# Kernel tuning notes

Measured on AMD Instinct MI355X. Metric: run time of the kernel, lower is better.

The kernel has to match this reference:

```python
import jax, jax.numpy as jnp
import numpy as np

N = 100000   # nodes
E = 800000   # edges
IN = 128     # in_dim
H = 256      # hidden
G = 512      # global cache rows


def _w(k, shape):
    fan_in = shape[0]
    return jax.random.normal(k, shape, jnp.float32) / np.sqrt(fan_in)


def setup_inputs() -> dict:
    key = jax.random.key(0)
    ks = jax.random.split(key, 24)
    x = jax.random.normal(ks[0], (N, IN), jnp.float32)
    edge_index = jax.random.randint(ks[1], (2, E), 0, N, jnp.int64)
    global_cache = jax.random.normal(ks[2], (G, H), jnp.float32)
    return {
        "x": x,
        "edge_index": edge_index,
        "global_cache": global_cache,
        "Wp": _w(ks[3], (IN, 64)), "bp": jnp.zeros((64,), jnp.float32),
        "W1l": _w(ks[4], (64, H)), "b1l": jnp.zeros((H,), jnp.float32),
        "W1r": _w(ks[5], (64, H)),
        "W2l": _w(ks[6], (H, H)), "b2l": jnp.zeros((H,), jnp.float32),
        "W2r": _w(ks[7], (H, H)),
        "Wq": _w(ks[8], (H, H)), "bq": jnp.zeros((H,), jnp.float32),
        "Wk": _w(ks[9], (H, H)), "bk": jnp.zeros((H,), jnp.float32),
        "Wv": _w(ks[10], (H, H)), "bv": jnp.zeros((H,), jnp.float32),
        "Wm1": _w(ks[11], (2 * H, H)), "bm1": jnp.zeros((H,), jnp.float32),
        "Wm2": _w(ks[12], (H, 2)), "bm2": jnp.zeros((2,), jnp.float32),
    }


def _sage(h, src, dst, Wl, bl, Wr):
    # PyG SAGEConv (mean aggr): lin_l(mean_{j in N(i)} h_j) + lin_r(h_i)
    agg = jax.ops.segment_sum(h[src], dst, num_segments=N)          # [N, d]
    cnt = jax.ops.segment_sum(jnp.ones((src.shape[0],), h.dtype), dst, num_segments=N)
    mean = agg / jnp.maximum(cnt, 1.0)[:, None]
    return mean @ Wl + bl + h @ Wr


def reference(x, edge_index, global_cache, Wp, bp, W1l, b1l, W1r,
              W2l, b2l, W2r, Wq, bq, Wk, bk, Wv, bv, Wm1, bm1, Wm2, bm2):
    src, dst = edge_index[0], edge_index[1]
    x_emb = jax.nn.relu(x @ Wp + bp)                                 # [N, 64]
    h = jax.nn.relu(_sage(x_emb, src, dst, W1l, b1l, W1r))           # [N, H]
    # dropout is identity in eval mode
    h = _sage(h, src, dst, W2l, b2l, W2r)                            # [N, H]
    # global attention
    Q = h @ Wq + bq                                                  # [N, H]
    K = global_cache @ Wk + bk                                       # [G, H]
    V = global_cache @ Wv + bv                                       # [G, H]
    attn = jax.nn.softmax(Q @ K.T / np.sqrt(H).astype(np.float32), axis=-1)  # [N, G]
    g = attn @ V                                                     # [N, H]
    h_cat = jnp.concatenate([h, g], axis=1)                          # [N, 2H]
    out = jax.nn.relu(h_cat @ Wm1 + bm1) @ Wm2 + bm2                 # [N, 2]
    return out
```

## Files before the change

kernel.cpp:

```cpp
#include <hip/hip_runtime.h>
#include <cstdint>
#include <cstddef>


#define NN 100000
#define NE 800000
#define CR 50000
#define NB1 98
#define CNTB 3125
#define XCVB 12500
#define NJOB 11
#define WCVB (NJOB * 32)
#define EMB_MB 782

typedef __attribute__((ext_vector_type(8))) short short8;
typedef __attribute__((ext_vector_type(8))) unsigned short ushort8;
typedef __attribute__((ext_vector_type(4))) float f32x4;

__device__ __forceinline__ float b2f(ushort u) {
  union { unsigned u; float f; } v; v.u = ((unsigned)u) << 16; return v.f;
}
__device__ __forceinline__ ushort f2b(float f) {
  union { float f; unsigned u; } v; v.f = f;
  unsigned r = v.u + 0x7FFFu + ((v.u >> 16) & 1u);
  return (ushort)(r >> 16);
}
__device__ __forceinline__ void gl_lds16(const void* g, void* l) {
  __builtin_amdgcn_global_load_lds((const __attribute__((address_space(1))) void*)g,
                                   (__attribute__((address_space(3))) void*)l, 16, 0, 0);
}

__global__ void zero_detect_k(const int* __restrict__ ei, int* __restrict__ flag,
                              int* __restrict__ cnt, int n) {
  if (blockIdx.x == 0) {
    __shared__ int ok;
    int t = threadIdx.x;
    if (t == 0) ok = 1;
    __syncthreads();
    if (ei[2 * t + 1] != 0) ok = 0;
    __syncthreads();
    if (t == 0) *flag = ok;
  } else {
    int i = (blockIdx.x - 1) * 256 + threadIdx.x;
    if (i < n) cnt[i] = 0;
  }
}

struct CvtJobs {
  const float* src[NJOB];
  ushort* dst[NJOB];
  int R[NJOB], C[NJOB], off[NJOB], tr[NJOB];
  float sc[NJOB];
};

__global__ void count_cvt_k(const int* __restrict__ ei, const int* __restrict__ flag,
                            int* __restrict__ cnt, int* __restrict__ loc,
                            const float* __restrict__ x, ushort* __restrict__ xb,
                            int E, int n4, CvtJobs jb) {
  int b = blockIdx.x;
  if (b < CNTB) {
    int i = b * 256 + threadIdx.x;
    if (i >= E) return;
    const bool i64 = (*flag != 0);
    unsigned d = (unsigned)(i64 ? ei[2 * E + 2 * i] : ei[E + i]);
    int p = -1;
    if (d < NN) p = atomicAdd(&cnt[d], 1);
    loc[i] = p;
  } else if (b < CNTB + XCVB) {
    int i = (b - CNTB) * 256 + threadIdx.x;
    if (i < n4) {
      float4 v = ((const float4*)x)[i];
      ushort4 o; o.x = f2b(v.x); o.y = f2b(v.y); o.z = f2b(v.z); o.w = f2b(v.w);
      ((ushort4*)xb)[i] = o;
    }
  } else {
    int wb = b - CNTB - XCVB;
    int j = wb >> 5;
    int ib = wb & 31;
    const int Cj = jb.C[j], Rj = jb.R[j];
    const float sc = jb.sc[j];
    const int n = Rj * Cj;
    if (jb.tr[j]) {
      for (int i = ib * 256 + threadIdx.x; i < n; i += 32 * 256) {
        int c = i / Rj, r = i - c * Rj;
        jb.dst[j][i] = f2b(jb.src[j][(size_t)(jb.off[j] + r) * Cj + c] * sc);
      }
    } else {
      for (int i = ib * 256 + threadIdx.x; i < n; i += 32 * 256)
        jb.dst[j][i] = f2b(jb.src[j][i] * sc);
    }
  }
}

__device__ __forceinline__ void scan1_body(const int* __restrict__ cnt,
                                           int* __restrict__ rowptr,
                                           int* __restrict__ bsum, int n, int b,
                                           char* smem) {
  int* ls = (int*)smem;
  const int t = threadIdx.x;
  const int base = b * 1024 + t * 4;
  int v[4]; int s = 0;
#pragma unroll
  for (int j = 0; j < 4; ++j) { int i = base + j; v[j] = (i < n) ? cnt[i] : 0; s += v[j]; }
  ls[t] = s; __syncthreads();
  int x = s;
  for (int o = 1; o < 256; o <<= 1) {
    int a = (t >= o) ? ls[t - o] : 0; __syncthreads();
    x += a; ls[t] = x; __syncthreads();
  }
  int run = x - s;
#pragma unroll
  for (int j = 0; j < 4; ++j) { run += v[j]; int i = base + j; if (i < n) rowptr[i + 1] = run; }
  if (t == 255) bsum[b] = x;
}

__device__ __forceinline__ void scan2_body(const int* __restrict__ bsum,
                                           int* __restrict__ boff, int nb,
                                           char* smem) {
  int* ls = (int*)smem;
  int t = threadIdx.x;
  int v = (t < 128 && t < nb) ? bsum[t] : 0;
  if (t < 128) ls[t] = v;
  __syncthreads();
  int x = v;
  for (int o = 1; o < 128; o <<= 1) {
    int a = (t < 128 && t >= o) ? ls[t - o] : 0;
    __syncthreads();
    x += a;
    if (t < 128) ls[t] = x;
    __syncthreads();
  }
  if (t < 128 && t < nb) boff[t] = x - v;
}

__device__ __forceinline__ void sbias_body(const float* __restrict__ bq,
                                           const ushort* __restrict__ Kmat,
                                           float* __restrict__ sbias, int blk) {
  int g = blk * 4 + (threadIdx.x >> 6);
  int lane = threadIdx.x & 63;
  if (g >= 512) return;
  ushort4 kv = ((const ushort4*)(Kmat + (size_t)g * 256))[lane];
  float4 bv = ((const float4*)bq)[lane];
  float p = b2f(kv.x) * bv.x + b2f(kv.y) * bv.y + b2f(kv.z) * bv.z + b2f(kv.w) * bv.w;
  for (int off = 32; off; off >>= 1) p += __shfl_xor(p, off);
  if (lane == 0) sbias[g] = p * 0.0625f;
}

__global__ void scan3_k(int* __restrict__ rowptr, const int* __restrict__ boff, int n) {
  int i = blockIdx.x * 256 + threadIdx.x;
  if (i == 0) rowptr[0] = 0;
  if (i < n) rowptr[i + 1] += boff[i >> 10];
}

__global__ void fill_edges_k(const int* __restrict__ ei, const int* __restrict__ flag,
                             const int* __restrict__ rowptr, const int* __restrict__ loc,
                             int* __restrict__ eidx, int E) {
  int i = blockIdx.x * 256 + threadIdx.x;
  if (i >= E) return;
  const bool i64 = (*flag != 0);
  unsigned s = (unsigned)(i64 ? ei[2 * i] : ei[i]);
  unsigned d = (unsigned)(i64 ? ei[2 * E + 2 * i] : ei[E + i]);
  int lc = loc[i];
  if (d < NN && s < NN && lc >= 0) {
    unsigned p = (unsigned)(rowptr[d] + lc);
    if (p < (unsigned)E) eidx[p] = (int)s;
  }
}

__global__ void agg64_k(const ushort* __restrict__ X, const int* __restrict__ rowptr,
                        const int* __restrict__ eidx, ushort* __restrict__ mean,
                        int r0, int M) {
  int nl = blockIdx.x * 4 + (threadIdx.x >> 6);
  int l = threadIdx.x & 63;
  int e4 = l >> 4;
  int d4 = l & 15;
  if (nl >= M) return;
  int node = r0 + nl;
  int s = rowptr[node], e = rowptr[node + 1];
  float a0 = 0.f, a1 = 0.f, a2 = 0.f, a3 = 0.f;
  for (int i = s + e4; i < e; i += 4) {
    unsigned sc = (unsigned)eidx[i];
    if (sc < NN) {
      ushort4 v = ((const ushort4*)(X + (size_t)sc * 64))[d4];
      a0 += b2f(v.x); a1 += b2f(v.y); a2 += b2f(v.z); a3 += b2f(v.w);
    }
  }
  a0 += __shfl_xor(a0, 16); a0 += __shfl_xor(a0, 32);
  a1 += __shfl_xor(a1, 16); a1 += __shfl_xor(a1, 32);
  a2 += __shfl_xor(a2, 16); a2 += __shfl_xor(a2, 32);
  a3 += __shfl_xor(a3, 16); a3 += __shfl_xor(a3, 32);
  if (e4 == 0) {
    float inv = 1.f / (float)max(e - s, 1);
    ushort4 o; o.x = f2b(a0 * inv); o.y = f2b(a1 * inv); o.z = f2b(a2 * inv); o.w = f2b(a3 * inv);
    ((ushort4*)(mean + (size_t)nl * 64))[d4] = o;
  }
}

__global__ void agg256_k(const ushort* __restrict__ X, const int* __restrict__ rowptr,
                         const int* __restrict__ eidx, ushort* __restrict__ mean,
                         int r0, int M) {
  int nl = blockIdx.x * 4 + (threadIdx.x >> 6);
  int l = threadIdx.x & 63;
  int g = l >> 5;
  int d = l & 31;
  if (nl >= M) return;
  int node = r0 + nl;
  int s = rowptr[node], e = rowptr[node + 1];
  float a[8], c[8];
#pragma unroll
  for (int k = 0; k < 8; ++k) { a[k] = 0.f; c[k] = 0.f; }
  for (int i = s + g; i < e; i += 4) {
    unsigned s0 = (unsigned)eidx[i];
    if (s0 < NN) {
      ushort8 v = *(const ushort8*)(X + (size_t)s0 * 256 + d * 8);
#pragma unroll
      for (int k = 0; k < 8; ++k) a[k] += b2f((ushort)v[k]);
    }
    int i2 = i + 2;
    if (i2 < e) {
      unsigned s1 = (unsigned)eidx[i2];
      if (s1 < NN) {
        ushort8 v = *(const ushort8*)(X + (size_t)s1 * 256 + d * 8);
#pragma unroll
        for (int k = 0; k < 8; ++k) c[k] += b2f((ushort)v[k]);
      }
    }
  }
  float inv = 1.f / (float)max(e - s, 1);
  ushort8 o;
#pragma unroll
  for (int k = 0; k < 8; ++k) {
    float t = a[k] + c[k];
    t += __shfl_xor(t, 32);
    o[k] = (short)f2b(t * inv);
  }
  if (g == 0) *(ushort8*)(mean + (size_t)nl * 256 + d * 8) = o;
}

template<int BN, bool RELU, bool OUTBF>
__device__ __forceinline__ void gemm_body(
    const ushort* __restrict__ A1, const ushort* __restrict__ BT1, int K1,
    const ushort* __restrict__ A2, const ushort* __restrict__ BT2, int K2,
    const float* __restrict__ bias, void* __restrict__ Cv, int M, int Nc,
    int bmi, int bni, char* smem) {
  constexpr int NR = BN / 32;
  constexpr int WTN = BN / 2;
  constexpr int ABYT = 128 * 64 * 2;
  constexpr int BBYT = BN * 64 * 2;
  constexpr int BUF = ABYT + BBYT;
  constexpr int CP = BN + 8;
  const int tid = threadIdx.x;
  const int l = tid & 63;
  const int w = tid >> 6;
  const int wm = w >> 1, wn = w & 1;
  const int bm = bmi * 128, bn = bni * BN;
  const int r15 = l & 15, g4 = l >> 4;

  const int nt1 = K1 >> 6;
  const int nt2 = A2 ? (K2 >> 6) : 0;
  const int nt = nt1 + nt2;

  auto STAGE = [&](int buf, int t) {
    const ushort* A = (t < nt1) ? A1 : A2;
    const ushort* BT = (t < nt1) ? BT1 : BT2;
    const int K = (t < nt1) ? K1 : K2;
    const int k0 = ((t < nt1) ? t : t - nt1) << 6;
    char* As = smem + buf * BUF;
    char* Bs = As + ABYT;
#pragma unroll
    for (int p = 0; p < 4; ++p) {
      int idx = tid + p * 256;
      int row = idx >> 3, slot = idx & 7;
      int kb = slot ^ (row & 7);
      int grow = bm + row; if (grow >= M) grow = M - 1;
      gl_lds16(A + (size_t)grow * K + k0 + kb * 8, As + idx * 16);
    }
#pragma unroll
    for (int p = 0; p < BN / 32; ++p) {
      int idx = tid + p * 256;
      int row = idx >> 3, slot = idx & 7;
      int kb = slot ^ (row & 7);
      gl_lds16(BT + (size_t)(bn + row) * K + k0 + kb * 8, Bs + idx * 16);
    }
  };

  f32x4 acc[4][NR];
  const f32x4 zz = {0.f, 0.f, 0.f, 0.f};
#pragma unroll
  for (int m = 0; m < 4; ++m)
#pragma unroll
    for (int n = 0; n < NR; ++n) acc[m][n] = zz;

  STAGE(0, 0);
  int cur = 0;
  for (int t = 0; t < nt; ++t) {
    __syncthreads();
    if (t + 1 < nt) STAGE(cur ^ 1, t + 1);
    const char* As = smem + cur * BUF;
    const char* Bs = As + ABYT;
#pragma unroll
    for (int s = 0; s < 2; ++s) {
      short8 a[4], b[NR];
      const int slotx = (((s * 4 + g4) ^ (r15 & 7)) << 4);
#pragma unroll
      for (int m = 0; m < 4; ++m) {
        int row = wm * 64 + m * 16 + r15;
        a[m] = *(const short8*)(As + row * 128 + slotx);
      }
#pragma unroll
      for (int n = 0; n < NR; ++n) {
        int row = wn * WTN + n * 16 + r15;
        b[n] = *(const short8*)(Bs + row * 128 + slotx);
      }
#pragma unroll
      for (int m = 0; m < 4; ++m)
#pragma unroll
        for (int n = 0; n < NR; ++n)
          acc[m][n] = __builtin_amdgcn_mfma_f32_16x16x32_bf16(a[m], b[n], acc[m][n], 0, 0, 0);
    }
    cur ^= 1;
  }
  __syncthreads();
  if (OUTBF) {
    ushort* Cs = (ushort*)smem;
#pragma unroll
    for (int n = 0; n < NR; ++n) {
      int col = wn * WTN + n * 16 + r15;
      float bv = bias ? bias[bn + col] : 0.f;
#pragma unroll
      for (int m = 0; m < 4; ++m) {
#pragma unroll
        for (int j = 0; j < 4; ++j) {
          int row = wm * 64 + m * 16 + g4 * 4 + j;
          float v = acc[m][n][j] + bv;
          if (RELU) v = fmaxf(v, 0.f);
          Cs[row * CP + col] = f2b(v);
        }
      }
    }
    __syncthreads();
    constexpr int C8 = BN / 8;
    for (int it = tid; it < 128 * C8; it += 256) {
      int row = it / C8, c8 = it % C8;
      if (bm + row < M)
        *(ushort8*)((ushort*)Cv + (size_t)(bm + row) * Nc + bn + c8 * 8) =
            *(const ushort8*)(Cs + row * CP + c8 * 8);
    }
  } else {
#pragma unroll
    for (int n = 0; n < NR; ++n) {
      int col = bn + wn * WTN + n * 16 + r15;
      float bv = bias ? bias[col] : 0.f;
#pragma unroll
      for (int m = 0; m < 4; ++m) {
#pragma unroll
        for (int j = 0; j < 4; ++j) {
          int row = bm + wm * 64 + m * 16 + g4 * 4 + j;
          if (row < M) {
            float v = acc[m][n][j] + bv;
            if (RELU) v = fmaxf(v, 0.f);
            ((float*)Cv)[(size_t)row * Nc + col] = v;
          }
        }
      }
    }
  }
}

template<int BN, bool RELU, bool OUTBF>
__global__ __launch_bounds__(256)
void mfma_gemm_k(const ushort* __restrict__ A1, const ushort* __restrict__ BT1, int K1,
                 const ushort* __restrict__ A2, const ushort* __restrict__ BT2, int K2,
                 const float* __restrict__ bias, void* __restrict__ Cv, int M, int Nc) {
  constexpr int BUF = 128 * 64 * 2 + BN * 64 * 2;
  constexpr int CP = BN + 8;
  constexpr int SZ_EPI = 128 * CP * 2;
  constexpr int SZ = (2 * BUF > SZ_EPI) ? 2 * BUF : SZ_EPI;
  __shared__ __align__(16) char smem[SZ];
  gemm_body<BN, RELU, OUTBF>(A1, BT1, K1, A2, BT2, K2, bias, Cv, M, Nc,
                             blockIdx.x, blockIdx.y, smem);
}

__global__ __launch_bounds__(256)
void stage2_k(const int* __restrict__ cnt, int* __restrict__ rowptr, int* __restrict__ bsum,
              const ushort* __restrict__ gcb, const ushort* __restrict__ WkT,
              const float* __restrict__ bk, ushort* __restrict__ Kmatb,
              const ushort* __restrict__ WvT, const float* __restrict__ bvv,
              ushort* __restrict__ Vmatb,
              const ushort* __restrict__ xb, const ushort* __restrict__ WpT,
              const float* __restrict__ bp, ushort* __restrict__ x_emb) {
  __shared__ __align__(16) char smem[65536];
  int b = blockIdx.x;
  if (b < 8) {
    gemm_body<128, false, true>(gcb, WkT, 256, nullptr, nullptr, 0, bk, Kmatb,
                                512, 256, b & 3, b >> 2, smem);
  } else if (b < 16) {
    int lb = b - 8;
    gemm_body<128, false, true>(gcb, WvT, 256, nullptr, nullptr, 0, bvv, Vmatb,
                                512, 256, lb & 3, lb >> 2, smem);
  } else if (b < 16 + EMB_MB) {
    gemm_body<64, true, true>(xb, WpT, 128, nullptr, nullptr, 0, bp, x_emb,
                              NN, 64, b - 16, 0, smem);
  } else {
    scan1_body(cnt, rowptr, bsum, NN, b - (16 + EMB_MB), smem);
  }
}

__global__ __launch_bounds__(256)
void stage3_k(const ushort* __restrict__ Kmatb, const ushort* __restrict__ Wqb,
              ushort* __restrict__ KWqT,
              const ushort* __restrict__ Wm1bT, const ushort* __restrict__ Vmatb,
              ushort* __restrict__ W_pvT,
              const float* __restrict__ bq, float* __restrict__ sbias,
              const int* __restrict__ bsum, int* __restrict__ boff) {
  __shared__ __align__(16) char smem[65536];
  int b = blockIdx.x;
  if (b < 8) {
    gemm_body<128, false, true>(Kmatb, Wqb, 256, nullptr, nullptr, 0, nullptr, KWqT,
                                512, 256, b & 3, b >> 2, smem);
  } else if (b < 16) {
    int lb = b - 8;
    gemm_body<128, false, true>(Wm1bT, Vmatb, 256, nullptr, nullptr, 0, nullptr, W_pvT,
                                256, 512, lb & 1, lb >> 1, smem);
  } else if (b < 144) {
    sbias_body(bq, Kmatb, sbias, b - 16);
  } else {
    scan2_body(bsum, boff, NB1, smem);
  }
}

__global__ __launch_bounds__(256)
void mlp_out_k(const ushort* __restrict__ A1, const ushort* __restrict__ BT1, int K1,
               const ushort* __restrict__ A2, const ushort* __restrict__ BT2, int K2,
               const float* __restrict__ bias, const float* __restrict__ Wm2,
               const float* __restrict__ bm2, float* __restrict__ out, int M) {
  constexpr int NR = 8;
  constexpr int WTN = 128;
  constexpr int ABYT = 64 * 32 * 2;
  constexpr int BBYT = 256 * 32 * 2;
  constexpr int BUF = ABYT + BBYT;
  __shared__ __align__(16) char smem[2 * BUF];
  const int tid = threadIdx.x;
  const int l = tid & 63;
  const int w = tid >> 6;
  const int wm = w >> 1, wn = w & 1;
  const int bm = blockIdx.x * 64;
  const int r15 = l & 15, g4 = l >> 4;

  const int nt1 = K1 >> 5;
  const int nt2 = K2 >> 5;
  const int nt = nt1 + nt2;

  auto STAGE = [&](int buf, int t) {
    const ushort* A = (t < nt1) ? A1 : A2;
    const ushort* BT = (t < nt1) ? BT1 : BT2;
    const int K = (t < nt1) ? K1 : K2;
    const int k0 = ((t < nt1) ? t : t - nt1) << 5;
    char* As = smem + buf * BUF;
    char* Bs = As + ABYT;
    {
      int row = tid >> 2, slot = tid & 3;
      int kb = slot ^ (row & 3);
      int grow = bm + row; if (grow >= M) grow = M - 1;
      gl_lds16(A + (size_t)grow * K + k0 + kb * 8, As + tid * 16);
    }
#pragma unroll
    for (int p = 0; p < 4; ++p) {
      int idx = tid + p * 256;
      int row = idx >> 2, slot = idx & 3;
      int kb = slot ^ (row & 3);
      gl_lds16(BT + (size_t)row * K + k0 + kb * 8, Bs + idx * 16);
    }
  };

  f32x4 acc[2][NR];
  const f32x4 zz = {0.f, 0.f, 0.f, 0.f};
#pragma unroll
  for (int m = 0; m < 2; ++m)
#pragma unroll
    for (int n = 0; n < NR; ++n) acc[m][n] = zz;

  STAGE(0, 0);
  int cur = 0;
  for (int t = 0; t < nt; ++t) {
    __syncthreads();
    if (t + 1 < nt) STAGE(cur ^ 1, t + 1);
    const char* As = smem + cur * BUF;
    const char* Bs = As + ABYT;
    short8 a[2], b[NR];
#pragma unroll
    for (int m = 0; m < 2; ++m) {
      int row = wm * 32 + m * 16 + r15;
      a[m] = *(const short8*)(As + row * 64 + ((g4 ^ (row & 3)) << 4));
    }
#pragma unroll
    for (int n = 0; n < NR; ++n) {
      int row = wn * WTN + n * 16 + r15;
      b[n] = *(const short8*)(Bs + row * 64 + ((g4 ^ (row & 3)) << 4));
    }
#pragma unroll
    for (int m = 0; m < 2; ++m)
#pragma unroll
      for (int n = 0; n < NR; ++n)
        acc[m][n] = __builtin_amdgcn_mfma_f32_16x16x32_bf16(a[m], b[n], acc[m][n], 0, 0, 0);
    cur ^= 1;
  }
  __syncthreads();
  float bv[NR], w20[NR], w21[NR];
#pragma unroll
  for (int n = 0; n < NR; ++n) {
    int col = wn * WTN + n * 16 + r15;
    bv[n] = bias[col];
    w20[n] = Wm2[col * 2 + 0];
    w21[n] = Wm2[col * 2 + 1];
  }
  float* red = (float*)smem;
#pragma unroll
  for (int m = 0; m < 2; ++m) {
#pragma unroll
    for (int j = 0; j < 4; ++j) {
      float p0 = 0.f, p1 = 0.f;
#pragma unroll
      for (int n = 0; n < NR; ++n) {
        float v = fmaxf(acc[m][n][j] + bv[n], 0.f);
        p0 += v * w20[n];
        p1 += v * w21[n];
      }
      p0 += __shfl_xor(p0, 1); p1 += __shfl_xor(p1, 1);
      p0 += __shfl_xor(p0, 2); p1 += __shfl_xor(p1, 2);
      p0 += __shfl_xor(p0, 4); p1 += __shfl_xor(p1, 4);
      p0 += __shfl_xor(p0, 8); p1 += __shfl_xor(p1, 8);
      if (r15 == 0) {
        int rl = wm * 32 + m * 16 + g4 * 4 + j;
        red[wn * 128 + rl * 2 + 0] = p0;
        red[wn * 128 + rl * 2 + 1] = p1;
      }
    }
  }
  __syncthreads();
  if (tid < 128) {
    int rl = tid >> 1, j = tid & 1;
    int row = bm + rl;
    if (row < M)
      out[(size_t)row * 2 + j] = red[rl * 2 + j] + red[128 + rl * 2 + j] + bm2[j];
  }
}

__global__ void softmax_k(ushort* __restrict__ SP, int M) {
  int row = blockIdx.x * 4 + (threadIdx.x >> 6);
  int lane = threadIdx.x & 63;
  if (row >= M) return;
  ushort4* p = (ushort4*)(SP + (size_t)row * 512);
  ushort4 ua = p[lane];
  ushort4 ub = p[lane + 64];
  float ax = b2f(ua.x), ay = b2f(ua.y), az = b2f(ua.z), aw = b2f(ua.w);
  float bx = b2f(ub.x), by = b2f(ub.y), bz = b2f(ub.z), bw = b2f(ub.w);
  float m = fmaxf(fmaxf(fmaxf(ax, ay), fmaxf(az, aw)),
                  fmaxf(fmaxf(bx, by), fmaxf(bz, bw)));
  for (int off = 32; off; off >>= 1) m = fmaxf(m, __shfl_xor(m, off));
  ax = expf(ax - m); ay = expf(ay - m); az = expf(az - m); aw = expf(aw - m);
  bx = expf(bx - m); by = expf(by - m); bz = expf(bz - m); bw = expf(bw - m);
  float s = ax + ay + az + aw + bx + by + bz + bw;
  for (int off = 32; off; off >>= 1) s += __shfl_xor(s, off);
  float inv = 1.f / s;
  ushort4 oa, ob;
  oa.x = f2b(ax * inv); oa.y = f2b(ay * inv); oa.z = f2b(az * inv); oa.w = f2b(aw * inv);
  ob.x = f2b(bx * inv); ob.y = f2b(by * inv); ob.z = f2b(bz * inv); ob.w = f2b(bw * inv);
  p[lane] = oa;
  p[lane + 64] = ob;
}

extern "C" void kernel_launch(void* const* d_in, const int* in_sizes, int n_in,
                              void* d_out, int out_size, void* d_ws, size_t ws_size,
                              hipStream_t stream) {
  const int N = NN, E = NE;
  const float* x   = (const float*)d_in[0];
  const int*   ei  = (const int*)d_in[1];
  const float* gc  = (const float*)d_in[2];
  const float* Wp  = (const float*)d_in[3];
  const float* bp  = (const float*)d_in[4];
  const float* W1l = (const float*)d_in[5];
  const float* b1l = (const float*)d_in[6];
  const float* W1r = (const float*)d_in[7];
  const float* W2l = (const float*)d_in[8];
  const float* b2l = (const float*)d_in[9];
  const float* W2r = (const float*)d_in[10];
  const float* Wq  = (const float*)d_in[11];
  const float* bq  = (const float*)d_in[12];
  const float* Wk  = (const float*)d_in[13];
  const float* bk  = (const float*)d_in[14];
  const float* Wv  = (const float*)d_in[15];
  const float* bv  = (const float*)d_in[16];
  const float* Wm1 = (const float*)d_in[17];
  const float* bm1 = (const float*)d_in[18];
  const float* Wm2 = (const float*)d_in[19];
  const float* bm2 = (const float*)d_in[20];
  float* out = (float*)d_out;

  char* base = (char*)d_ws;
  size_t off = 0;
  auto take = [&](size_t bytes) -> void* {
    void* r = base + off;
    off += (bytes + 255) & ~(size_t)255;
    return r;
  };
  int* cnt    = (int*)take((size_t)N * 4);
  int* rowptr = (int*)take((size_t)(N + 1) * 4);
  int* loc    = (int*)take((size_t)E * 4);
  int* eidx   = (int*)take((size_t)E * 4);
  int* eflag  = (int*)take(256);
  int* bsum   = (int*)take(NB1 * 4);
  int* boff   = (int*)take(NB1 * 4);
  ushort* WpT   = (ushort*)take((size_t)64 * 128 * 2);
  ushort* W1lT  = (ushort*)take((size_t)256 * 64 * 2);
  ushort* W1rT  = (ushort*)take((size_t)256 * 64 * 2);
  ushort* W2lT  = (ushort*)take((size_t)256 * 256 * 2);
  ushort* W2rT  = (ushort*)take((size_t)256 * 256 * 2);
  ushort* WkT   = (ushort*)take((size_t)256 * 256 * 2);
  ushort* WvT   = (ushort*)take((size_t)256 * 256 * 2);
  ushort* Wqb   = (ushort*)take((size_t)256 * 256 * 2);
  ushort* Wm1aT = (ushort*)take((size_t)256 * 256 * 2);
  ushort* Wm1bT = (ushort*)take((size_t)256 * 256 * 2);
  ushort* gcb   = (ushort*)take((size_t)512 * 256 * 2);
  ushort* Kmatb = (ushort*)take((size_t)512 * 256 * 2);
  ushort* Vmatb = (ushort*)take((size_t)512 * 256 * 2);
  ushort* W_pvT = (ushort*)take((size_t)256 * 512 * 2);
  ushort* KWqT  = (ushort*)take((size_t)512 * 256 * 2);
  float*  sbias = (float*)take((size_t)512 * 4);
  const size_t szU_pre = (size_t)N * 128 * 2 + (size_t)N * 64 * 2 + (size_t)N * 64 * 2;
  const size_t szU_chunk = (size_t)CR * 2048;
  char* U = (char*)take(szU_pre > szU_chunk ? szU_pre : szU_chunk);
  ushort* h = (ushort*)take((size_t)N * 256 * 2);
  if (off > ws_size) return;

  ushort* xb    = (ushort*)U;
  ushort* x_emb = (ushort*)(U + (size_t)N * 128 * 2);
  ushort* mean1 = (ushort*)(U + (size_t)N * 128 * 2 + (size_t)N * 64 * 2);
  ushort* mean2_c  = (ushort*)U;
  ushort* h2_c     = (ushort*)(U + (size_t)CR * 512);
  ushort* SP_c     = (ushort*)(U + (size_t)CR * 1024);

  const int MB = (N + 127) / 128;
  const int n4 = N * 128 / 4;
  dim3 thr(256);

  CvtJobs jb;
  {
    const float* s_[NJOB] = {gc, Wq, Wp, W1l, W1r, W2l, W2r, Wk, Wv, Wm1, Wm1};
    ushort* d_[NJOB] = {gcb, Wqb, WpT, W1lT, W1rT, W2lT, W2rT, WkT, WvT, Wm1aT, Wm1bT};
    int R_[NJOB] = {512, 256, 128, 64, 64, 256, 256, 256, 256, 256, 256};
    int C_[NJOB] = {256, 256, 64, 256, 256, 256, 256, 256, 256, 256, 256};
    int o_[NJOB] = {0, 0, 0, 0, 0, 0, 0, 0, 0, 0, 256};
    int t_[NJOB] = {0, 0, 1, 1, 1, 1, 1, 1, 1, 1, 1};
    for (int j = 0; j < NJOB; ++j) {
      jb.src[j] = s_[j]; jb.dst[j] = d_[j]; jb.R[j] = R_[j]; jb.C[j] = C_[j];
      jb.off[j] = o_[j]; jb.tr[j] = t_[j]; jb.sc[j] = (j == 1) ? 0.0625f : 1.0f;
    }
  }

  zero_detect_k<<<1 + (N + 255) / 256, thr, 0, stream>>>(ei, eflag, cnt, N);
  count_cvt_k<<<CNTB + XCVB + WCVB, thr, 0, stream>>>(ei, eflag, cnt, loc, x, xb, E, n4, jb);
  stage2_k<<<16 + EMB_MB + NB1, thr, 0, stream>>>(
      cnt, rowptr, bsum, gcb, WkT, bk, Kmatb, WvT, bv, Vmatb, xb, WpT, bp, x_emb);
  stage3_k<<<145, thr, 0, stream>>>(
      Kmatb, Wqb, KWqT, Wm1bT, Vmatb, W_pvT, bq, sbias, bsum, boff);
  scan3_k<<<(N + 255) / 256, thr, 0, stream>>>(rowptr, boff, N);
  fill_edges_k<<<(E + 255) / 256, thr, 0, stream>>>(ei, eflag, rowptr, loc, eidx, E);

  agg64_k<<<(N + 3) / 4, thr, 0, stream>>>(x_emb, rowptr, eidx, mean1, 0, N);
  mfma_gemm_k<128, true, true><<<dim3(MB, 2), thr, 0, stream>>>(
      mean1, W1lT, 64, x_emb, W1rT, 64, b1l, h, N, 256);

  for (int r0 = 0; r0 < N; r0 += CR) {
    const int CRc = (N - r0 < CR) ? (N - r0) : CR;
    const int MBc = (CRc + 127) / 128;
    const int MBc64 = (CRc + 63) / 64;
    agg256_k<<<(CRc + 3) / 4, thr, 0, stream>>>(h, rowptr, eidx, mean2_c, r0, CRc);
    mfma_gemm_k<128, false, true><<<dim3(MBc, 2), thr, 0, stream>>>(
        mean2_c, W2lT, 256, h + (size_t)r0 * 256, W2rT, 256, b2l, h2_c, CRc, 256);
    mfma_gemm_k<128, false, true><<<dim3(MBc, 4), thr, 0, stream>>>(
        h2_c, KWqT, 256, nullptr, nullptr, 0, sbias, SP_c, CRc, 512);
    softmax_k<<<(CRc + 3) / 4, thr, 0, stream>>>(SP_c, CRc);
    mlp_out_k<<<dim3(MBc64, 1), thr, 0, stream>>>(
        h2_c, Wm1aT, 256, SP_c, W_pvT, 512, bm1, Wm2, bm2, out + (size_t)r0 * 2, CRc);
  }
}
```

Baseline: 477.4 us.

## Fuse softmax into MLP output kernel via per-row max/sum prepass

Removes the standalone softmax kernel and instead computes row max and inverse sum inside mlp_out_k in a prologue that reads each 512-wide score row. The A2 tile staging then applies exp and normalization on the fly via synchronous loads instead of async global-to-LDS copies. This avoids a read-modify-write pass over the score matrix and one launch per chunk, but reads scores twice in the prologue, recomputes exp during staging, and loses async loads for that operand.

```diff
diff --git a/kernel.cpp b/kernel.cpp
--- a/kernel.cpp
+++ b/kernel.cpp
@@ -440,6 +440,7 @@
   constexpr int BBYT = 256 * 32 * 2;
   constexpr int BUF = ABYT + BBYT;
   __shared__ __align__(16) char smem[2 * BUF];
+  __shared__ float mrow[64], linv[64];
   const int tid = threadIdx.x;
   const int l = tid & 63;
   const int w = tid >> 6;
@@ -451,8 +452,31 @@
   const int nt2 = K2 >> 5;
   const int nt = nt1 + nt2;
 
+  {
+    int row = tid >> 2, q = tid & 3;
+    int gr = bm + row; if (gr >= M) gr = M - 1;
+    const ushort8* sp = (const ushort8*)(A2 + (size_t)gr * K2 + q * 128);
+    float mx = -1e30f;
+    for (int i = 0; i < 16; ++i) {
+      ushort8 v = sp[i];
+#pragma unroll
+      for (int k = 0; k < 8; ++k) mx = fmaxf(mx, b2f((ushort)v[k]));
+    }
+    mx = fmaxf(mx, __shfl_xor(mx, 1));
+    mx = fmaxf(mx, __shfl_xor(mx, 2));
+    float sum = 0.f;
+    for (int i = 0; i < 16; ++i) {
+      ushort8 v = sp[i];
+#pragma unroll
+      for (int k = 0; k < 8; ++k) sum += expf(b2f((ushort)v[k]) - mx);
+    }
+    sum += __shfl_xor(sum, 1);
+    sum += __shfl_xor(sum, 2);
+    if (q == 0) { mrow[row] = mx; linv[row] = 1.f / sum; }
+  }
+  __syncthreads();
+
   auto STAGE = [&](int buf, int t) {
-    const ushort* A = (t < nt1) ? A1 : A2;
     const ushort* BT = (t < nt1) ? BT1 : BT2;
     const int K = (t < nt1) ? K1 : K2;
     const int k0 = ((t < nt1) ? t : t - nt1) << 5;
@@ -462,7 +486,17 @@
       int row = tid >> 2, slot = tid & 3;
       int kb = slot ^ (row & 3);
       int grow = bm + row; if (grow >= M) grow = M - 1;
-      gl_lds16(A + (size_t)grow * K + k0 + kb * 8, As + tid * 16);
+      if (t < nt1) {
+        gl_lds16(A1 + (size_t)grow * K + k0 + kb * 8, As + tid * 16);
+      } else {
+        ushort8 v = *(const ushort8*)(A2 + (size_t)grow * K + k0 + kb * 8);
+        float m = mrow[row], li = linv[row];
+        ushort8 o;
+#pragma unroll
+        for (int k = 0; k < 8; ++k)
+          o[k] = (short)f2b(expf(b2f((ushort)v[k]) - m) * li);
+        *(ushort8*)(As + tid * 16) = o;
+      }
     }
 #pragma unroll
     for (int p = 0; p < 4; ++p) {
@@ -544,30 +578,6 @@
     if (row < M)
       out[(size_t)row * 2 + j] = red[rl * 2 + j] + red[128 + rl * 2 + j] + bm2[j];
   }
-}
-
-__global__ void softmax_k(ushort* __restrict__ SP, int M) {
-  int row = blockIdx.x * 4 + (threadIdx.x >> 6);
-  int lane = threadIdx.x & 63;
-  if (row >= M) return;
-  ushort4* p = (ushort4*)(SP + (size_t)row * 512);
-  ushort4 ua = p[lane];
-  ushort4 ub = p[lane + 64];
-  float ax = b2f(ua.x), ay = b2f(ua.y), az = b2f(ua.z), aw = b2f(ua.w);
-  float bx = b2f(ub.x), by = b2f(ub.y), bz = b2f(ub.z), bw = b2f(ub.w);
-  float m = fmaxf(fmaxf(fmaxf(ax, ay), fmaxf(az, aw)),
-                  fmaxf(fmaxf(bx, by), fmaxf(bz, bw)));
-  for (int off = 32; off; off >>= 1) m = fmaxf(m, __shfl_xor(m, off));
-  ax = expf(ax - m); ay = expf(ay - m); az = expf(az - m); aw = expf(aw - m);
-  bx = expf(bx - m); by = expf(by - m); bz = expf(bz - m); bw = expf(bw - m);
-  float s = ax + ay + az + aw + bx + by + bz + bw;
-  for (int off = 32; off; off >>= 1) s += __shfl_xor(s, off);
-  float inv = 1.f / s;
-  ushort4 oa, ob;
-  oa.x = f2b(ax * inv); oa.y = f2b(ay * inv); oa.z = f2b(az * inv); oa.w = f2b(aw * inv);
-  ob.x = f2b(bx * inv); ob.y = f2b(by * inv); ob.z = f2b(bz * inv); ob.w = f2b(bw * inv);
-  p[lane] = oa;
-  p[lane + 64] = ob;
 }
 
 extern "C" void kernel_launch(void* const* d_in, const int* in_sizes, int n_in,
@@ -680,7 +690,6 @@
         mean2_c, W2lT, 256, h + (size_t)r0 * 256, W2rT, 256, b2l, h2_c, CRc, 256);
     mfma_gemm_k<128, false, true><<<dim3(MBc, 4), thr, 0, stream>>>(
         h2_c, KWqT, 256, nullptr, nullptr, 0, sbias, SP_c, CRc, 512);
-    softmax_k<<<(CRc + 3) / 4, thr, 0, stream>>>(SP_c, CRc);
     mlp_out_k<<<dim3(MBc64, 1), thr, 0, stream>>>(
         h2_c, Wm1aT, 256, SP_c, W_pvT, 512, bm1, Wm2, bm2, out + (size_t)r0 * 2, CRc);
   }
```

Measured after the change: 524.9 us. +10.0%, slower.

## Replace 128x128 GEMM tiles with 64x256 tiles covering full output width

Applied to the files above, without the earlier changes.

Adds a new bf16 MFMA GEMM kernel with 64-row by 256-column block tiles and a 32-wide K step, double-buffered through LDS with XOR swizzle, and a staged bf16 epilogue written as 16-byte stores. It replaces the generic 128x128 gemm for the SAGE layer and Q·K score GEMMs. A single block now spans the full 256-wide output, so each A tile is read once instead of once per column block, and there are more, smaller row blocks. In exchange, more weight data is loaded per block and the smaller K step means more synchronisation rounds.

```diff
diff --git a/kernel.cpp b/kernel.cpp
--- a/kernel.cpp
+++ b/kernel.cpp
@@ -367,18 +367,108 @@
   }
 }
 
-template<int BN, bool RELU, bool OUTBF>
+template<bool RELU>
 __global__ __launch_bounds__(256)
-void mfma_gemm_k(const ushort* __restrict__ A1, const ushort* __restrict__ BT1, int K1,
-                 const ushort* __restrict__ A2, const ushort* __restrict__ BT2, int K2,
-                 const float* __restrict__ bias, void* __restrict__ Cv, int M, int Nc) {
-  constexpr int BUF = 128 * 64 * 2 + BN * 64 * 2;
-  constexpr int CP = BN + 8;
-  constexpr int SZ_EPI = 128 * CP * 2;
-  constexpr int SZ = (2 * BUF > SZ_EPI) ? 2 * BUF : SZ_EPI;
-  __shared__ __align__(16) char smem[SZ];
-  gemm_body<BN, RELU, OUTBF>(A1, BT1, K1, A2, BT2, K2, bias, Cv, M, Nc,
-                             blockIdx.x, blockIdx.y, smem);
+void gemm64_k(const ushort* __restrict__ A1, const ushort* __restrict__ BT1, int K1,
+              const ushort* __restrict__ A2, const ushort* __restrict__ BT2, int K2,
+              const float* __restrict__ bias, ushort* __restrict__ C, int M, int Nc) {
+  constexpr int NR = 8;
+  constexpr int WTN = 128;
+  constexpr int ABYT = 64 * 32 * 2;
+  constexpr int BBYT = 256 * 32 * 2;
+  constexpr int BUF = ABYT + BBYT;
+  constexpr int CP = 256 + 8;
+  __shared__ __align__(16) char smem[2 * BUF];
+  const int tid = threadIdx.x;
+  const int l = tid & 63;
+  const int w = tid >> 6;
+  const int wm = w >> 1, wn = w & 1;
+  const int bm = blockIdx.x * 64;
+  const int bn = blockIdx.y * 256;
+  const int r15 = l & 15, g4 = l >> 4;
+
+  const int nt1 = K1 >> 5;
+  const int nt2 = A2 ? (K2 >> 5) : 0;
+  const int nt = nt1 + nt2;
+
+  auto STAGE = [&](int buf, int t) {
+    const ushort* A = (t < nt1) ? A1 : A2;
+    const ushort* BT = (t < nt1) ? BT1 : BT2;
+    const int K = (t < nt1) ? K1 : K2;
+    const int k0 = ((t < nt1) ? t : t - nt1) << 5;
+    char* As = smem + buf * BUF;
+    char* Bs = As + ABYT;
+    {
+      int row = tid >> 2, slot = tid & 3;
+      int kb = slot ^ (row & 3);
+      int grow = bm + row; if (grow >= M) grow = M - 1;
+      gl_lds16(A + (size_t)grow * K + k0 + kb * 8, As + tid * 16);
+    }
+#pragma unroll
+    for (int p = 0; p < 4; ++p) {
+      int idx = tid + p * 256;
+      int row = idx >> 2, slot = idx & 3;
+      int kb = slot ^ (row & 3);
+      gl_lds16(BT + (size_t)(bn + row) * K + k0 + kb * 8, Bs + idx * 16);
+    }
+  };
+
+  f32x4 acc[2][NR];
+  const f32x4 zz = {0.f, 0.f, 0.f, 0.f};
+#pragma unroll
+  for (int m = 0; m < 2; ++m)
+#pragma unroll
+    for (int n = 0; n < NR; ++n) acc[m][n] = zz;
+
+  STAGE(0, 0);
+  int cur = 0;
+  for (int t = 0; t < nt; ++t) {
+    __syncthreads();
+    if (t + 1 < nt) STAGE(cur ^ 1, t + 1);
+    const char* As = smem + cur * BUF;
+    const char* Bs = As + ABYT;
+    short8 a[2], b[NR];
+#pragma unroll
+    for (int m = 0; m < 2; ++m) {
+      int row = wm * 32 + m * 16 + r15;
+      a[m] = *(const short8*)(As + row * 64 + ((g4 ^ (row & 3)) << 4));
+    }
+#pragma unroll
+    for (int n = 0; n < NR; ++n) {
+      int row = wn * WTN + n * 16 + r15;
+      b[n] = *(const short8*)(Bs + row * 64 + ((g4 ^ (row & 3)) << 4));
+    }
+#pragma unroll
+    for (int m = 0; m < 2; ++m)
+#pragma unroll
+      for (int n = 0; n < NR; ++n)
+        acc[m][n] = __builtin_amdgcn_mfma_f32_16x16x32_bf16(a[m], b[n], acc[m][n], 0, 0, 0);
+    cur ^= 1;
+  }
+  __syncthreads();
+  ushort* Cs = (ushort*)smem;
+#pragma unroll
+  for (int n = 0; n < NR; ++n) {
+    int col = wn * WTN + n * 16 + r15;
+    float bv = bias ? bias[bn + col] : 0.f;
+#pragma unroll
+    for (int m = 0; m < 2; ++m) {
+#pragma unroll
+      for (int j = 0; j < 4; ++j) {
+        int row = wm * 32 + m * 16 + g4 * 4 + j;
+        float v = acc[m][n][j] + bv;
+        if (RELU) v = fmaxf(v, 0.f);
+        Cs[row * CP + col] = f2b(v);
+      }
+    }
+  }
+  __syncthreads();
+  for (int it = tid; it < 64 * 32; it += 256) {
+    int row = it >> 5, c8 = it & 31;
+    if (bm + row < M)
+      *(ushort8*)(C + (size_t)(bm + row) * Nc + bn + c8 * 8) =
+          *(const ushort8*)(Cs + row * CP + c8 * 8);
+  }
 }
 
 __global__ __launch_bounds__(256)
@@ -640,7 +730,6 @@
   ushort* h2_c     = (ushort*)(U + (size_t)CR * 512);
   ushort* SP_c     = (ushort*)(U + (size_t)CR * 1024);
 
-  const int MB = (N + 127) / 128;
   const int n4 = N * 128 / 4;
   dim3 thr(256);
 
@@ -668,17 +757,16 @@
   fill_edges_k<<<(E + 255) / 256, thr, 0, stream>>>(ei, eflag, rowptr, loc, eidx, E);
 
   agg64_k<<<(N + 3) / 4, thr, 0, stream>>>(x_emb, rowptr, eidx, mean1, 0, N);
-  mfma_gemm_k<128, true, true><<<dim3(MB, 2), thr, 0, stream>>>(
+  gemm64_k<true><<<dim3((N + 63) / 64, 1), thr, 0, stream>>>(
       mean1, W1lT, 64, x_emb, W1rT, 64, b1l, h, N, 256);
 
   for (int r0 = 0; r0 < N; r0 += CR) {
     const int CRc = (N - r0 < CR) ? (N - r0) : CR;
-    const int MBc = (CRc + 127) / 128;
     const int MBc64 = (CRc + 63) / 64;
     agg256_k<<<(CRc + 3) / 4, thr, 0, stream>>>(h, rowptr, eidx, mean2_c, r0, CRc);
-    mfma_gemm_k<128, false, true><<<dim3(MBc, 2), thr, 0, stream>>>(
+    gemm64_k<false><<<dim3(MBc64, 1), thr, 0, stream>>>(
         mean2_c, W2lT, 256, h + (size_t)r0 * 256, W2rT, 256, b2l, h2_c, CRc, 256);
-    mfma_gemm_k<128, false, true><<<dim3(MBc, 4), thr, 0, stream>>>(
+    gemm64_k<false><<<dim3(MBc64, 2), thr, 0, stream>>>(
         h2_c, KWqT, 256, nullptr, nullptr, 0, sbias, SP_c, CRc, 512);
     softmax_k<<<(CRc + 3) / 4, thr, 0, stream>>>(SP_c, CRc);
     mlp_out_k<<<dim3(MBc64, 1), thr, 0, stream>>>(
```

After: 471.9 us. Within noise of the previous version (-1.2%).
